# Performance work log

Measured on AMD Instinct MI355X. Metric: run time of the kernel, lower is better.

## Reference

```python
import jax, jax.numpy as jnp
import numpy as np

BLOCK = 4  # block_size from init_kwargs


def space_to_channel_3d(x, b):
    # Faithful translation of SpaceToChannel_3d.forward (torch split/stack/permute chain).
    B, C, W, H, D = x.shape
    y = x.transpose(0, 2, 3, 4, 1)                      # (B, W, H, D, C)
    y = y.reshape(B, W, H, D // b, b, C)                # split depth into D//b chunks of b
    y = y.transpose(0, 3, 1, 2, 4, 5)                   # (B, D//b, W, H, b, C)
    y = y.reshape(B, D // b, W // b, H // b, C * b * b * b)  # per-chunk row-major reshape
    y = y.transpose(0, 2, 3, 1, 4)                      # (B, W//b, H//b, D//b, C*b^3)
    return y.transpose(0, 4, 1, 2, 3)                   # (B, C*b^3, W//b, H//b, D//b)


def channel_to_space_3d(x, b):
    # Faithful translation of ChannelToSpace_3d.forward.
    B, Cd, wd, hd, dd = x.shape
    b3 = b * b * b
    Cs = Cd // b3
    y = x.transpose(0, 2, 3, 4, 1)                      # (B, wd, hd, dd, Cd)
    y = y.reshape(B, wd, hd, dd, b * b, b, Cs)          # split b^3 dim into b^2 chunks of b
    y = y.transpose(0, 4, 1, 2, 3, 5, 6)                # (B, b^2, wd, hd, dd, b, Cs)
    y = y.reshape(B, b * b, wd, hd, dd * b, Cs)         # merge (dd, b) per chunk
    y = y.transpose(0, 2, 1, 3, 4, 5)                   # (B, wd, b^2, hd, dd*b, Cs)
    y = y.reshape(B, wd * b, hd * b, dd * b, Cs)        # row-major merge of (wd, b^2, hd)
    return y.transpose(0, 4, 1, 2, 3)                   # (B, Cs, wd*b, hd*b, dd*b)


def setup_inputs() -> dict:
    key = jax.random.key(0)
    k1, k2 = jax.random.split(key)
    x = jax.random.normal(k1, (4, 32, 64, 64, 64), dtype=jnp.float32)
    gamma = jax.random.normal(k2, (1,), dtype=jnp.float32)
    return {"x": x, "gamma": gamma}


def reference(x, gamma):
    b = BLOCK
    y = space_to_channel_3d(x, b)                       # (B, C*b^3, w, h, d)
    B, C, w, h, d = y.shape
    q = y.reshape(B, C, w * h * d)                      # (B, C', N)
    # channel-wise attention: energy (B, C', C')
    energy = jnp.einsum('bcn,ben->bce', q, q)
    energy_new = jnp.max(energy, axis=-1, keepdims=True) - energy
    attention = jax.nn.softmax(energy_new, axis=-1)
    out = jnp.einsum('bce,ben->bcn', attention, q)      # (B, C', N)
    out = out.reshape(B, C, w, h, d)
    out = gamma * out + y
    return channel_to_space_3d(out, b)
```

## Files before the change

kernel.cpp:

```cpp
#include <hip/hip_runtime.h>

typedef _Float16 f16;
typedef __attribute__((ext_vector_type(8))) _Float16 f16x8;
typedef __attribute__((ext_vector_type(4))) float f32x4;

#define CCH 2048
#define NSP 4096
#define NB  4

#define VMCNT8 asm volatile("s_waitcnt vmcnt(8)" ::: "memory")
#define VMCNT4 asm volatile("s_waitcnt vmcnt(4)" ::: "memory")
#define VMCNT0 asm volatile("s_waitcnt vmcnt(0)" ::: "memory")
#define CFENCE asm volatile("" ::: "memory")

__device__ __forceinline__ void gld16(const void* g, void* l) {
  __builtin_amdgcn_global_load_lds(
      (const __attribute__((address_space(1))) void*)g,
      (__attribute__((address_space(3))) void*)l, 16, 0, 0);
}

__global__ void pack_kernel(const float* __restrict__ x, f16* __restrict__ qh,
                            f16* __restrict__ ql, int b0) {
  int gid = blockIdx.x * 256 + threadIdx.x;
  int n = gid & (NSP - 1);
  int t = gid >> 12;
  int c = t & 31; t >>= 5;
  int r = t & 15; int ib = t >> 4;
  int wc = n >> 8, hc = (n >> 4) & 15, dc = n & 15;
  int w = wc * 4 + (hc >> 2);
  int h = (hc & 3) * 16 + r;
  int b = b0 + ib;
  const f32x4 v = *(const f32x4*)(x + ((((size_t)b * 32 + c) * 64 + w) * 64 + h) * 64 + dc * 4);
#pragma unroll
  for (int bd = 0; bd < 4; ++bd) {
    int cc = r * 128 + bd * 32 + c;
    size_t o = ((size_t)ib * CCH + cc) * NSP + n;
    float val = v[bd];
    f16 hi = (f16)val;
    qh[o] = hi;
    ql[o] = (f16)(val - (float)hi);
  }
}

__global__ void transpose_kernel(const f16* __restrict__ qh, f16* __restrict__ qhT) {
  int ib = blockIdx.z;
  int j0 = blockIdx.x * 64, n0 = blockIdx.y * 64;
  __shared__ f16 tile[64][72];
  int t = threadIdx.x;
  int r = t >> 3;
  int cb = (t & 7) * 8;
#pragma unroll
  for (int half = 0; half < 2; ++half) {
    int rr = r + half * 32;
    f16x8 v = *(const f16x8*)(qh + ((size_t)ib * CCH + j0 + rr) * NSP + n0 + cb);
    *(f16x8*)&tile[rr][cb] = v;
  }
  __syncthreads();
#pragma unroll
  for (int half = 0; half < 2; ++half) {
    int rr = r + half * 32;
    f16x8 o;
#pragma unroll
    for (int u = 0; u < 8; ++u) o[u] = tile[cb + u][rr];
    *(f16x8*)(qhT + ((size_t)ib * NSP + n0 + rr) * CCH + j0 + cb) = o;
  }
}

__global__ __launch_bounds__(256) void gemm1_kernel(const f16* __restrict__ qh,
                                                    const f16* __restrict__ ql,
                                                    float* __restrict__ energy) {
  int ib = blockIdx.z;
  int bx = blockIdx.x;
  int tri = (bx & 7) * 17 + (bx >> 3);
  int rem = tri, bi = 0, span = 16;
  while (rem >= span) { rem -= span; ++bi; --span; }
  int bj = bi + rem;
  int i0 = bi * 128, j0 = bj * 128;
  float* eout = energy + (size_t)ib * CCH * CCH;

  __shared__ f16 Lds[4][2][128 * 32];
  int tid = threadIdx.x;
  int lane = tid & 63, wv = tid >> 6;
  int l15 = lane & 15, quad = lane >> 4;
  int wr = (wv >> 1) * 64, wcol = (wv & 1) * 64;
  int swz = (l15 >> 1) & 3;
  int kbs = (lane & 3) ^ ((lane >> 3) & 3);

  int arr = wv >> 1, rh = wv & 1;
  int rbase = arr ? j0 : i0;
  size_t rowoff = ((size_t)ib * CCH + rbase + rh * 64 + (lane >> 2)) * NSP + kbs * 8;
  const f16* gqh = qh + rowoff;
  const f16* gql = ql + rowoff;

  auto stage = [&](int slot, int q) {
    const f16* src = arr ? (((q >> 7) == 1) ? gql : gqh)
                         : (((q >> 7) == 2) ? gql : gqh);
    int kk = (q & 127) << 5;
#pragma unroll
    for (int t = 0; t < 4; ++t)
      gld16(src + (size_t)(t * 16) * NSP + kk,
            &Lds[slot][arr][(rh * 64 + t * 16) * 32]);
  };

  const f32x4 vzero = {0.f, 0.f, 0.f, 0.f};
  f32x4 acc[4][4];
#pragma unroll
  for (int a = 0; a < 4; ++a)
#pragma unroll
    for (int bq = 0; bq < 4; ++bq) acc[a][bq] = vzero;

  const int NP = 3 * (NSP / 32);
  stage(0, 0); stage(1, 1); stage(2, 2);
  for (int p = 0; p < NP; ++p) {
    int remp = NP - 1 - p;
    if (remp >= 2) { VMCNT8; } else if (remp == 1) { VMCNT4; } else { VMCNT0; }
    __builtin_amdgcn_s_barrier();
    CFENCE;
    if (p + 3 < NP) stage((p + 3) & 3, p + 3);
    int s = p & 3;
    const f16* As = &Lds[s][0][0];
    const f16* Bs = &Lds[s][1][0];
    f16x8 ah[4], bh[4];
#pragma unroll
    for (int mt = 0; mt < 4; ++mt)
      ah[mt] = *(const f16x8*)&As[(wr + mt * 16 + l15) * 32 + ((quad ^ swz) * 8)];
#pragma unroll
    for (int nt = 0; nt < 4; ++nt)
      bh[nt] = *(const f16x8*)&Bs[(wcol + nt * 16 + l15) * 32 + ((quad ^ swz) * 8)];
    __builtin_amdgcn_s_setprio(1);
#pragma unroll
    for (int mt = 0; mt < 4; ++mt)
#pragma unroll
      for (int nt = 0; nt < 4; ++nt)
        acc[mt][nt] = __builtin_amdgcn_mfma_f32_16x16x32_f16(ah[mt], bh[nt], acc[mt][nt], 0, 0, 0);
    __builtin_amdgcn_s_setprio(0);
  }
  bool diag = (bi == bj);
#pragma unroll
  for (int mt = 0; mt < 4; ++mt)
#pragma unroll
    for (int nt = 0; nt < 4; ++nt)
#pragma unroll
      for (int rg = 0; rg < 4; ++rg) {
        int row = i0 + wr + mt * 16 + quad * 4 + rg;
        int col = j0 + wcol + nt * 16 + l15;
        float v = acc[mt][nt][rg];
        eout[(size_t)row * CCH + col] = v;
        if (!diag) eout[(size_t)col * CCH + row] = v;
      }
}

__global__ void softmax_kernel(const float* __restrict__ e0,
                               const float* __restrict__ gamma_p,
                               f16* __restrict__ attn) {
  int i = blockIdx.x, ib = blockIdx.y;
  const float* r0 = e0 + ((size_t)ib * CCH + i) * CCH;
  f16* arow = attn + ((size_t)ib * CCH + i) * CCH;
  int t = threadIdx.x;
  f32x4 v0 = *(const f32x4*)(r0 + t * 8);
  f32x4 v1 = *(const f32x4*)(r0 + t * 8 + 4);
  float m = v0[0];
#pragma unroll
  for (int u = 1; u < 4; ++u) m = fminf(m, v0[u]);
#pragma unroll
  for (int u = 0; u < 4; ++u) m = fminf(m, v1[u]);
#pragma unroll
  for (int off = 32; off > 0; off >>= 1) m = fminf(m, __shfl_xor(m, off));
  __shared__ float redA[4], redB[4];
  if ((t & 63) == 0) redA[t >> 6] = m;
  __syncthreads();
  m = fminf(fminf(redA[0], redA[1]), fminf(redA[2], redA[3]));
  float e[8], s = 0.f;
#pragma unroll
  for (int u = 0; u < 4; ++u) { e[u] = __expf(m - v0[u]); s += e[u]; }
#pragma unroll
  for (int u = 0; u < 4; ++u) { e[4 + u] = __expf(m - v1[u]); s += e[4 + u]; }
#pragma unroll
  for (int off = 32; off > 0; off >>= 1) s += __shfl_xor(s, off);
  if ((t & 63) == 0) redB[t >> 6] = s;
  __syncthreads();
  s = redB[0] + redB[1] + redB[2] + redB[3];
  float gamma = *gamma_p;
  float ginv = gamma / s;
  int du = i - t * 8;
  f16x8 o;
#pragma unroll
  for (int u = 0; u < 8; ++u) {
    float v = e[u] * ginv;
    if (u == du) v += 1.0f;
    o[u] = (f16)v;
  }
  *(f16x8*)(arow + t * 8) = o;
}

__global__ __launch_bounds__(256) void gemm2_kernel(const f16* __restrict__ attn,
                                                    const f16* __restrict__ qhT,
                                                    float* __restrict__ out, int b0) {
  int ib = blockIdx.z;
  int lin = blockIdx.x + gridDim.x * blockIdx.y;
  int nwg = gridDim.x * gridDim.y;
  int cpx = nwg >> 3;
  int lin2 = (lin & 7) * cpx + (lin >> 3);
  int i0 = (lin2 & 15) * 128;
  int n0 = (lin2 >> 4) * 128;
  __shared__ f16 Lds[4][2][128 * 32];
  int tid = threadIdx.x;
  int lane = tid & 63, wv = tid >> 6;
  int l15 = lane & 15, quad = lane >> 4;
  int wr = (wv >> 1) * 64, wcol = (wv & 1) * 64;
  int swz = (l15 >> 1) & 3;
  int kbs = (lane & 3) ^ ((lane >> 3) & 3);

  int arr = wv >> 1, rh = wv & 1;
  const f16* gbase = arr ? (qhT + ((size_t)ib * NSP + n0) * CCH)
                         : (attn + ((size_t)ib * CCH + i0) * CCH);
  const f16* gsrc = gbase + (size_t)(rh * 64 + (lane >> 2)) * CCH + kbs * 8;

  auto stage = [&](int slot, int kk) {
#pragma unroll
    for (int t = 0; t < 4; ++t)
      gld16(gsrc + (size_t)(t * 16) * CCH + kk,
            &Lds[slot][arr][(rh * 64 + t * 16) * 32]);
  };

  const f32x4 vzero = {0.f, 0.f, 0.f, 0.f};
  f32x4 acc[4][4];
#pragma unroll
  for (int a = 0; a < 4; ++a)
#pragma unroll
    for (int bq = 0; bq < 4; ++bq) acc[a][bq] = vzero;

  const int NP = CCH / 32;
  stage(0, 0); stage(1, 32); stage(2, 64);
  for (int p = 0; p < NP; ++p) {
    int remp = NP - 1 - p;
    if (remp >= 2) { VMCNT8; } else if (remp == 1) { VMCNT4; } else { VMCNT0; }
    __builtin_amdgcn_s_barrier();
    CFENCE;
    if (p + 3 < NP) stage((p + 3) & 3, (p + 3) << 5);
    int s = p & 3;
    const f16* As = &Lds[s][0][0];
    const f16* Bs = &Lds[s][1][0];
    f16x8 af[4], bf[4];
#pragma unroll
    for (int mt = 0; mt < 4; ++mt)
      af[mt] = *(const f16x8*)&As[(wr + mt * 16 + l15) * 32 + ((quad ^ swz) * 8)];
#pragma unroll
    for (int nt = 0; nt < 4; ++nt)
      bf[nt] = *(const f16x8*)&Bs[(wcol + nt * 16 + l15) * 32 + ((quad ^ swz) * 8)];
    __builtin_amdgcn_s_setprio(1);
#pragma unroll
    for (int mt = 0; mt < 4; ++mt)
#pragma unroll
      for (int nt = 0; nt < 4; ++nt)
        acc[mt][nt] = __builtin_amdgcn_mfma_f32_16x16x32_f16(af[mt], bf[nt], acc[mt][nt], 0, 0, 0);
    __builtin_amdgcn_s_setprio(0);
  }

  __syncthreads();
  float* eld = (float*)&Lds[0][0][0];
#pragma unroll
  for (int mt = 0; mt < 4; ++mt) {
    int f = (wr >> 5) + (mt >> 1);
    int gb = (mt & 1) * 16 + quad * 4;
#pragma unroll
    for (int nt = 0; nt < 4; ++nt) {
      int jh = (wcol >> 4) + nt;
#pragma unroll
      for (int rg = 0; rg < 4; ++rg)
        eld[(gb + rg) * 512 + jh * 64 + l15 * 4 + f] = acc[mt][nt][rg];
    }
  }
  __syncthreads();
  int b = b0 + ib;
  int e = i0 >> 7;
  int iw = n0 >> 8;
  int W = iw * 4 + (e >> 2);
  int H0 = (e & 3) * 16 + ((n0 >> 4) & 15);
#pragma unroll
  for (int u = 0; u < 8; ++u) {
    int g = wv * 8 + u;
    size_t goff = ((((size_t)b * 32 + g) * 64 + W) * 4096) + (size_t)H0 * 64;
#pragma unroll
    for (int hv = 0; hv < 2; ++hv) {
      int fo = hv * 256 + lane * 4;
      *(f32x4*)(out + goff + fo) = *(const f32x4*)&eld[g * 512 + fo];
    }
  }
}

extern "C" void kernel_launch(void* const* d_in, const int* in_sizes, int n_in,
                              void* d_out, int out_size, void* d_ws, size_t ws_size,
                              hipStream_t stream) {
  const float* x = (const float*)d_in[0];
  const float* gamma = (const float*)d_in[1];
  float* out = (float*)d_out;

  const size_t szQ = (size_t)CCH * NSP;
  const size_t szE = (size_t)CCH * CCH;

  const size_t pb = szQ * 2 * 3 + szE * 4 + szE * 2;

  int nb = (ws_size >= (size_t)NB * pb) ? NB : 1;

  char* p = (char*)d_ws;
  f16* qh = (f16*)p;   p += (size_t)nb * szQ * 2;
  f16* ql = (f16*)p;   p += (size_t)nb * szQ * 2;
  f16* qhT = (f16*)p;  p += (size_t)nb * szQ * 2;
  float* energy = (float*)p; p += (size_t)nb * szE * 4;
  f16* attn = (f16*)p;

  for (int b0 = 0; b0 < NB; b0 += nb) {
    pack_kernel<<<nb * 8192, 256, 0, stream>>>(x, qh, ql, b0);
    transpose_kernel<<<dim3(32, 64, nb), 256, 0, stream>>>(qh, qhT);
    gemm1_kernel<<<dim3(136, 1, nb), 256, 0, stream>>>(qh, ql, energy);
    softmax_kernel<<<dim3(CCH, nb), 256, 0, stream>>>(energy, gamma, attn);
    gemm2_kernel<<<dim3(16, 32, nb), 256, 0, stream>>>(attn, qhT, out, b0);
  }
}
```

Baseline: 841.6 us.

## Restructure gemm1 split-precision loop to load hi/lo tiles once per K step

The energy GEMM previously ran three sequential K passes (hi*hi, hi*lo, lo*hi), reloading the hi operands for each pass. It now stages the hi and lo tiles of both operands together for each K chunk and issues all three MFMAs per fragment in one pass, which cuts global and LDS traffic for the hi operands. The block grows to 512 threads (8 waves, each owning a 64x32 tile) and the pipeline drops from 4 to 3 stages. The larger LDS footprint and block size may limit how many blocks fit per CU.

```diff
diff --git a/kernel.cpp b/kernel.cpp
--- a/kernel.cpp
+++ b/kernel.cpp
@@ -66,7 +66,7 @@
   }
 }
 
-__global__ __launch_bounds__(256) void gemm1_kernel(const f16* __restrict__ qh,
+__global__ __launch_bounds__(512) void gemm1_kernel(const f16* __restrict__ qh,
                                                     const f16* __restrict__ ql,
                                                     float* __restrict__ energy) {
   int ib = blockIdx.z;
@@ -78,68 +78,78 @@
   int i0 = bi * 128, j0 = bj * 128;
   float* eout = energy + (size_t)ib * CCH * CCH;
 
-  __shared__ f16 Lds[4][2][128 * 32];
+  __shared__ f16 Lds[3][4][128 * 32];
   int tid = threadIdx.x;
   int lane = tid & 63, wv = tid >> 6;
   int l15 = lane & 15, quad = lane >> 4;
-  int wr = (wv >> 1) * 64, wcol = (wv & 1) * 64;
+  int wr = (wv >> 2) * 64, wcol = (wv & 3) * 32;
   int swz = (l15 >> 1) & 3;
   int kbs = (lane & 3) ^ ((lane >> 3) & 3);
 
   int arr = wv >> 1, rh = wv & 1;
-  int rbase = arr ? j0 : i0;
-  size_t rowoff = ((size_t)ib * CCH + rbase + rh * 64 + (lane >> 2)) * NSP + kbs * 8;
-  const f16* gqh = qh + rowoff;
-  const f16* gql = ql + rowoff;
-
-  auto stage = [&](int slot, int q) {
-    const f16* src = arr ? (((q >> 7) == 1) ? gql : gqh)
-                         : (((q >> 7) == 2) ? gql : gqh);
-    int kk = (q & 127) << 5;
+  int rbase = (arr < 2) ? i0 : j0;
+  const f16* srcq = (arr & 1) ? ql : qh;
+  const f16* gsrc = srcq + ((size_t)ib * CCH + rbase + rh * 64 + (lane >> 2)) * NSP + kbs * 8;
+
+  auto stage = [&](int slot, int kk) {
 #pragma unroll
     for (int t = 0; t < 4; ++t)
-      gld16(src + (size_t)(t * 16) * NSP + kk,
+      gld16(gsrc + (size_t)(t * 16) * NSP + kk,
             &Lds[slot][arr][(rh * 64 + t * 16) * 32]);
   };
 
   const f32x4 vzero = {0.f, 0.f, 0.f, 0.f};
-  f32x4 acc[4][4];
+  f32x4 acc[4][2];
 #pragma unroll
   for (int a = 0; a < 4; ++a)
 #pragma unroll
-    for (int bq = 0; bq < 4; ++bq) acc[a][bq] = vzero;
-
-  const int NP = 3 * (NSP / 32);
-  stage(0, 0); stage(1, 1); stage(2, 2);
+    for (int bq = 0; bq < 2; ++bq) acc[a][bq] = vzero;
+
+  const int NP = NSP / 32;
+  stage(0, 0); stage(1, 32);
+  int s = 0;
   for (int p = 0; p < NP; ++p) {
-    int remp = NP - 1 - p;
-    if (remp >= 2) { VMCNT8; } else if (remp == 1) { VMCNT4; } else { VMCNT0; }
+    if (p < NP - 1) { VMCNT4; } else { VMCNT0; }
     __builtin_amdgcn_s_barrier();
     CFENCE;
-    if (p + 3 < NP) stage((p + 3) & 3, p + 3);
-    int s = p & 3;
-    const f16* As = &Lds[s][0][0];
-    const f16* Bs = &Lds[s][1][0];
-    f16x8 ah[4], bh[4];
+    if (p + 2 < NP) {
+      int ns = s + 2; if (ns >= 3) ns -= 3;
+      stage(ns, (p + 2) << 5);
+    }
+    const f16* Ah = &Lds[s][0][0];
+    const f16* Al = &Lds[s][1][0];
+    const f16* Bh = &Lds[s][2][0];
+    const f16* Bl = &Lds[s][3][0];
+    f16x8 ah[4], al[4], bh[2], bl[2];
+#pragma unroll
+    for (int mt = 0; mt < 4; ++mt) {
+      int row = wr + mt * 16 + l15;
+      ah[mt] = *(const f16x8*)&Ah[row * 32 + ((quad ^ swz) * 8)];
+      al[mt] = *(const f16x8*)&Al[row * 32 + ((quad ^ swz) * 8)];
+    }
+#pragma unroll
+    for (int nt = 0; nt < 2; ++nt) {
+      int col = wcol + nt * 16 + l15;
+      bh[nt] = *(const f16x8*)&Bh[col * 32 + ((quad ^ swz) * 8)];
+      bl[nt] = *(const f16x8*)&Bl[col * 32 + ((quad ^ swz) * 8)];
+    }
+    __builtin_amdgcn_s_setprio(1);
 #pragma unroll
     for (int mt = 0; mt < 4; ++mt)
-      ah[mt] = *(const f16x8*)&As[(wr + mt * 16 + l15) * 32 + ((quad ^ swz) * 8)];
-#pragma unroll
-    for (int nt = 0; nt < 4; ++nt)
-      bh[nt] = *(const f16x8*)&Bs[(wcol + nt * 16 + l15) * 32 + ((quad ^ swz) * 8)];
-    __builtin_amdgcn_s_setprio(1);
-#pragma unroll
-    for (int mt = 0; mt < 4; ++mt)
-#pragma unroll
-      for (int nt = 0; nt < 4; ++nt)
+#pragma unroll
+      for (int nt = 0; nt < 2; ++nt) {
         acc[mt][nt] = __builtin_amdgcn_mfma_f32_16x16x32_f16(ah[mt], bh[nt], acc[mt][nt], 0, 0, 0);
+        acc[mt][nt] = __builtin_amdgcn_mfma_f32_16x16x32_f16(ah[mt], bl[nt], acc[mt][nt], 0, 0, 0);
+        acc[mt][nt] = __builtin_amdgcn_mfma_f32_16x16x32_f16(al[mt], bh[nt], acc[mt][nt], 0, 0, 0);
+      }
     __builtin_amdgcn_s_setprio(0);
+    s = (s == 2) ? 0 : s + 1;
   }
   bool diag = (bi == bj);
 #pragma unroll
   for (int mt = 0; mt < 4; ++mt)
 #pragma unroll
-    for (int nt = 0; nt < 4; ++nt)
+    for (int nt = 0; nt < 2; ++nt)
 #pragma unroll
       for (int rg = 0; rg < 4; ++rg) {
         int row = i0 + wr + mt * 16 + quad * 4 + rg;
@@ -313,7 +323,7 @@
   for (int b0 = 0; b0 < NB; b0 += nb) {
     pack_kernel<<<nb * 8192, 256, 0, stream>>>(x, qh, ql, b0);
     transpose_kernel<<<dim3(32, 64, nb), 256, 0, stream>>>(qh, qhT);
-    gemm1_kernel<<<dim3(136, 1, nb), 256, 0, stream>>>(qh, ql, energy);
+    gemm1_kernel<<<dim3(136, 1, nb), 512, 0, stream>>>(qh, ql, energy);
     softmax_kernel<<<dim3(CCH, nb), 256, 0, stream>>>(energy, gamma, attn);
     gemm2_kernel<<<dim3(16, 32, nb), 256, 0, stream>>>(attn, qhT, out, b0);
   }
```

Result: faster. 751.8 us (-10.7%).
